# Kernel tuning notes

Hardware: AMD Instinct MI355X
Metric: run time of the kernel (lower is better)

Reference implementation:

```python
import jax, jax.numpy as jnp
import numpy as np

# Module config (init_kwargs)
K_PERIODS = 5
PMAX = 512
MIN_PERIOD_THRESHOLD = 2

B, T, N = 32, 2048, 128


def setup_inputs() -> dict:
    key = jax.random.key(0)
    x = jax.random.normal(key, (B, T, N), dtype=jnp.float32)
    return {"x": x}


def reference(x):
    """Faithful dense/padded JAX version of PeriodicityTransform.forward (mask=None).

    The torch module emits ragged PeriodGroups keyed by (cycles, period).
    Since jit requires static shapes, we return the same per-(series, freq)
    information in padded form:
      tiles   : [BN, K, T]  flattened folded tile (row-major cycle x period),
                 zero-padded past take = cycles*periods
      periods : [BN, K] int32
      cycles  : [BN, K] int32
    tiles[bn,k,:take].reshape(cycles, period) equals the torch tile exactly.
    """
    Bq, Tq, Nq = x.shape
    BN = Bq * Nq
    seqs = jnp.transpose(x, (0, 2, 1)).reshape(BN, Tq)  # [BN, T]

    # --- _topk_freq ---
    spec = jnp.fft.rfft(seqs, axis=-1)                   # [BN, T//2+1]
    mag2 = spec.real ** 2 + spec.imag ** 2
    mag2 = mag2.at[..., 0].set(0.0)                      # kill DC
    k = min(K_PERIODS, mag2.shape[-1] - 1)
    _, kidx = jax.lax.top_k(mag2, k)                     # [BN, K]
    kidx = jnp.maximum(kidx, 1).astype(jnp.int32)

    # --- period / cycle computation (valid_lengths == T, no mask) ---
    lengths = jnp.int32(Tq)
    periods = lengths // kidx                            # [BN, K]
    periods = jnp.minimum(periods, PMAX)
    min_period = min(MIN_PERIOD_THRESHOLD, Tq)
    periods = jnp.maximum(periods, min_period)
    periods = jnp.maximum(periods, 1)
    cycles = jnp.maximum(lengths // periods, 1)          # [BN, K]

    take = cycles * periods                              # [BN, K], <= T
    t = jnp.arange(Tq, dtype=jnp.int32)                  # [T]
    start = Tq - take                                    # [BN, K]
    gather_idx = jnp.clip(start[..., None] + t, 0, Tq - 1)  # [BN, K, T]
    valid = t[None, None, :] < take[..., None]           # [BN, K, T]

    src = jnp.broadcast_to(seqs[:, None, :], (BN, k, Tq))
    tiles = jnp.take_along_axis(src, gather_idx, axis=-1)
    tiles = jnp.where(valid, tiles, jnp.zeros((), dtype=tiles.dtype))
    return tiles, periods, cycles
```

## Files before the change

kernel.cpp:

```cpp
#include <hip/hip_runtime.h>

#define B_ 32
#define T_ 2048
#define N_ 128
#define K_ 5
#define BN_ (B_ * N_)
#define PMAX_ 512
#define MINP_ 2

static constexpr double PI_D = 3.14159265358979323846264338327950288;
static constexpr double S2_D = 0.70710678118654752440084436210485;

struct cd { double r, i; };

__device__ __forceinline__ void bf_w(cd& u, cd& v, double wr, double wi) {
    const double tr = v.r * wr - v.i * wi;
    const double ti = v.r * wi + v.i * wr;
    v.r = u.r - tr; v.i = u.i - ti;
    u.r += tr;      u.i += ti;
}
__device__ __forceinline__ void bf_1(cd& u, cd& v) {
    const double tr = v.r, ti = v.i;
    v.r = u.r - tr; v.i = u.i - ti;
    u.r += tr;      u.i += ti;
}
__device__ __forceinline__ void bf_mi(cd& u, cd& v) {
    const double tr = v.i, ti = -v.r;
    v.r = u.r - tr; v.i = u.i - ti;
    u.r += tr;      u.i += ti;
}
__device__ __forceinline__ int sw(int i) { return i ^ ((i >> 5) & 31); }

__global__ __launch_bounds__(256) void pt_twiddle(double2* __restrict__ tw) {
    const int m = blockIdx.x * 256 + threadIdx.x;
    if (m < 1024) {
        double s, c;
        sincos(-2.0 * PI_D * (double)m / 2048.0, &s, &c);
        tw[m] = make_double2(c, s);
    }
}

__global__ __launch_bounds__(256, 4) void pt_fft_tiles(const float* __restrict__ x,
                                                       float* __restrict__ out,
                                                       const double2* __restrict__ tw) {
    __shared__ double re[2048];
    __shared__ double im[2048];
    __shared__ double redv[8];
    __shared__ int    redi[8];
    __shared__ int    win2[2];
    __shared__ int    sh_take[2][K_];

    const int i0  = blockIdx.x;
    const int q   = ((i0 & 7) << 8) | (i0 >> 3);
    const int bn0 = q * 2;
    const int b   = bn0 >> 7;
    const int n   = bn0 & 127;
    const int tid = threadIdx.x;

    const float* xp = x + (size_t)b * T_ * N_ + n;
    float2 v[8];
#pragma unroll
    for (int m = 0; m < 8; ++m)
        v[m] = *(const float2*)(xp + (size_t)(tid + 256 * m) * N_);

#pragma unroll
    for (int m = 0; m < 8; ++m) {
        const int t = tid + 256 * m;
        const int p = sw((int)(__brev((unsigned)t) >> 21));
        re[p] = (double)v[m].x;
        im[p] = (double)v[m].y;
    }
    __syncthreads();

    {
        const int base = tid * 8;
        cd E[8];
#pragma unroll
        for (int j = 0; j < 8; ++j) { const int p = sw(base + j); E[j].r = re[p]; E[j].i = im[p]; }
        bf_1(E[0], E[1]); bf_1(E[2], E[3]); bf_1(E[4], E[5]); bf_1(E[6], E[7]);
        bf_1(E[0], E[2]); bf_mi(E[1], E[3]); bf_1(E[4], E[6]); bf_mi(E[5], E[7]);
        bf_1(E[0], E[4]); bf_w(E[1], E[5], S2_D, -S2_D);
        bf_mi(E[2], E[6]); bf_w(E[3], E[7], -S2_D, -S2_D);
#pragma unroll
        for (int j = 0; j < 8; ++j) { const int p = sw(base + j); re[p] = E[j].r; im[p] = E[j].i; }
    }
    __syncthreads();

#pragma unroll
    for (int r = 0; r < 2; ++r) {
        const int s    = 4 + 3 * r;
        const int h    = 1 << (s - 1);
        const int bq   = tid & (h - 1);
        const int g    = tid >> (s - 1);
        const int base = g * 8 * h + bq;
        const double2 w1  = tw[bq << (11 - s)];
        const double2 w2a = tw[bq << (10 - s)];
        const double2 w2b = tw[(bq + h) << (10 - s)];
        const double2 w30 = tw[bq << (9 - s)];
        const double2 w31 = tw[(bq + h) << (9 - s)];
        const double2 w32 = tw[(bq + 2 * h) << (9 - s)];
        const double2 w33 = tw[(bq + 3 * h) << (9 - s)];
        cd E[8];
#pragma unroll
        for (int j = 0; j < 8; ++j) { const int p = sw(base + j * h); E[j].r = re[p]; E[j].i = im[p]; }
        bf_w(E[0], E[1], w1.x, w1.y);   bf_w(E[2], E[3], w1.x, w1.y);
        bf_w(E[4], E[5], w1.x, w1.y);   bf_w(E[6], E[7], w1.x, w1.y);
        bf_w(E[0], E[2], w2a.x, w2a.y); bf_w(E[1], E[3], w2b.x, w2b.y);
        bf_w(E[4], E[6], w2a.x, w2a.y); bf_w(E[5], E[7], w2b.x, w2b.y);
        bf_w(E[0], E[4], w30.x, w30.y); bf_w(E[1], E[5], w31.x, w31.y);
        bf_w(E[2], E[6], w32.x, w32.y); bf_w(E[3], E[7], w33.x, w33.y);
#pragma unroll
        for (int j = 0; j < 8; ++j) { const int p = sw(base + j * h); re[p] = E[j].r; im[p] = E[j].i; }
        __syncthreads();
    }

#pragma unroll
    for (int u = 0; u < 2; ++u) {
        const int bb = tid + 256 * u;
        const double2 wA = tw[bb << 1];
        const double2 wB = tw[bb];
        const double2 wC = tw[bb + 512];
        const int p0 = sw(bb), p1 = sw(bb + 512), p2 = sw(bb + 1024), p3 = sw(bb + 1536);
        cd E0 = {re[p0], im[p0]}, E1 = {re[p1], im[p1]};
        cd E2 = {re[p2], im[p2]}, E3 = {re[p3], im[p3]};
        bf_w(E0, E1, wA.x, wA.y); bf_w(E2, E3, wA.x, wA.y);
        bf_w(E0, E2, wB.x, wB.y); bf_w(E1, E3, wC.x, wC.y);
        re[p0] = E0.r; im[p0] = E0.i; re[p1] = E1.r; im[p1] = E1.i;
        re[p2] = E2.r; im[p2] = E2.i; re[p3] = E3.r; im[p3] = E3.i;
    }
    __syncthreads();

    double magsA[4], magsB[4];
#pragma unroll
    for (int m = 0; m < 4; ++m) {
        const int k  = 1 + tid + 256 * m;
        const int nk = 2048 - k;
        const int pk = sw(k), pn = sw(nk);
        const double zr = re[pk], zi = im[pk];
        const double yr = re[pn], yi = im[pn];
        const double ar = zr + yr, ai = zi - yi;
        const double br = zi + yi, bi = yr - zr;
        magsA[m] = ar * ar + ai * ai;
        magsB[m] = br * br + bi * bi;
    }

    const int wid  = tid >> 6;
    const int lane = tid & 63;
    for (int it = 0; it < K_; ++it) {
        double bvA = -1.0; int biA = 1 << 30;
        double bvB = -1.0; int biB = 1 << 30;
#pragma unroll
        for (int m = 0; m < 4; ++m) {
            const int k = 1 + tid + 256 * m;
            if (magsA[m] > bvA || (magsA[m] == bvA && k < biA)) { bvA = magsA[m]; biA = k; }
            if (magsB[m] > bvB || (magsB[m] == bvB && k < biB)) { bvB = magsB[m]; biB = k; }
        }
#pragma unroll
        for (int off = 32; off > 0; off >>= 1) {
            double v2 = __shfl_down(bvA, off); int i2 = __shfl_down(biA, off);
            if (v2 > bvA || (v2 == bvA && i2 < biA)) { bvA = v2; biA = i2; }
            v2 = __shfl_down(bvB, off); i2 = __shfl_down(biB, off);
            if (v2 > bvB || (v2 == bvB && i2 < biB)) { bvB = v2; biB = i2; }
        }
        if (lane == 0) {
            redv[wid] = bvA; redi[wid] = biA;
            redv[4 + wid] = bvB; redi[4 + wid] = biB;
        }
        __syncthreads();
        if (tid < 2) {
            const int base = 4 * tid;
            double vb = redv[base]; int ib = redi[base];
#pragma unroll
            for (int w = 1; w < 4; ++w) {
                const double v1 = redv[base + w]; const int i1 = redi[base + w];
                if (v1 > vb || (v1 == vb && i1 < ib)) { vb = v1; ib = i1; }
            }
            win2[tid] = ib;
            int period = T_ / ib;
            if (period > PMAX_) period = PMAX_;
            if (period < MINP_) period = MINP_;
            const int cyc = T_ / period;
            sh_take[tid][it] = (period << 16) | (period * cyc);
        }
        __syncthreads();
        const int wA = win2[0], wB = win2[1];
#pragma unroll
        for (int m = 0; m < 4; ++m) {
            const int k = 1 + tid + 256 * m;
            if (k == wA) magsA[m] = -1.0;
            if (k == wB) magsB[m] = -1.0;
        }
    }

    const size_t TILES = (size_t)BN_ * K_ * T_;
    if (tid < 2 * K_) {
        const int s2 = tid / K_, k2 = tid % K_;
        const int pk   = sh_take[s2][k2];
        const int per  = pk >> 16;
        const int take = pk & 0xFFFF;
        out[TILES + (size_t)(bn0 + s2) * K_ + k2]                      = (float)per;
        out[TILES + (size_t)BN_ * K_ + (size_t)(bn0 + s2) * K_ + k2]   = (float)(take / per);
    }

    float* rowA = out + (size_t)bn0 * (K_ * T_);
#pragma unroll
    for (int s2 = 0; s2 < 2; ++s2) {
#pragma unroll
        for (int k = 0; k < K_; ++k) {
            const int take  = sh_take[s2][k] & 0xFFFF;
            const int start = T_ - take;
            float* dst = rowA + (size_t)(s2 * K_ + k) * T_;
#pragma unroll
            for (int m = 0; m < 8; ++m) {
                const int t   = tid + 256 * m;
                const bool lo = (t < start);
                const int p   = lo ? (t + take) : (t - start);
                const float val = lo ? 0.0f : (s2 ? v[m].y : v[m].x);
                __builtin_nontemporal_store(val, dst + p);
            }
        }
    }
}

extern "C" void kernel_launch(void* const* d_in, const int* in_sizes, int n_in,
                              void* d_out, int out_size, void* d_ws, size_t ws_size,
                              hipStream_t stream) {
    const float* x = (const float*)d_in[0];
    float* out = (float*)d_out;
    double2* tw = (double2*)d_ws;

    pt_twiddle<<<dim3(4), dim3(256), 0, stream>>>(tw);
    pt_fft_tiles<<<dim3(BN_ / 2), dim3(256), 0, stream>>>(x, out, tw);
}
```

Before: 237.8 us.

## Compute per-wave top-K candidates locally and merge once, removing per-iteration barriers

Instead of a block-wide argmax with two barriers per top-K iteration, each wavefront independently extracts its own top-5 candidates via shuffles and writes them to shared memory. Two threads then merge the 4x5 candidates per series to pick the global top-5. This removes ten __syncthreads in exchange for a small serial merge on two threads. The merge relies on the global top-5 always being contained in the union of the per-wave top-5 lists.

Measured after the change: 247.6 us. +4.1%, slower.

```diff
diff --git a/kernel.cpp b/kernel.cpp
--- a/kernel.cpp
+++ b/kernel.cpp
@@ -45,9 +45,8 @@
                                                        const double2* __restrict__ tw) {
     __shared__ double re[2048];
     __shared__ double im[2048];
-    __shared__ double redv[8];
-    __shared__ int    redi[8];
-    __shared__ int    win2[2];
+    __shared__ double wcv[2][4][K_];
+    __shared__ int    wck[2][4][K_];
     __shared__ int    sh_take[2][K_];
 
     const int i0  = blockIdx.x;
@@ -146,6 +145,7 @@
 
     const int wid  = tid >> 6;
     const int lane = tid & 63;
+#pragma unroll
     for (int it = 0; it < K_; ++it) {
         double bvA = -1.0; int biA = 1 << 30;
         double bvB = -1.0; int biB = 1 << 30;
@@ -162,35 +162,48 @@
             v2 = __shfl_down(bvB, off); i2 = __shfl_down(biB, off);
             if (v2 > bvB || (v2 == bvB && i2 < biB)) { bvB = v2; biB = i2; }
         }
+        const double wvA = __shfl(bvA, 0); const int wiA = __shfl(biA, 0);
+        const double wvB = __shfl(bvB, 0); const int wiB = __shfl(biB, 0);
         if (lane == 0) {
-            redv[wid] = bvA; redi[wid] = biA;
-            redv[4 + wid] = bvB; redi[4 + wid] = biB;
-        }
-        __syncthreads();
-        if (tid < 2) {
-            const int base = 4 * tid;
-            double vb = redv[base]; int ib = redi[base];
-#pragma unroll
-            for (int w = 1; w < 4; ++w) {
-                const double v1 = redv[base + w]; const int i1 = redi[base + w];
-                if (v1 > vb || (v1 == vb && i1 < ib)) { vb = v1; ib = i1; }
+            wcv[0][wid][it] = wvA; wck[0][wid][it] = wiA;
+            wcv[1][wid][it] = wvB; wck[1][wid][it] = wiB;
+        }
+#pragma unroll
+        for (int m = 0; m < 4; ++m) {
+            const int k = 1 + tid + 256 * m;
+            if (k == wiA) magsA[m] = -1.0;
+            if (k == wiB) magsB[m] = -1.0;
+        }
+    }
+    __syncthreads();
+
+    if (tid < 2) {
+        double cv[20]; int ck[20];
+#pragma unroll
+        for (int w = 0; w < 4; ++w)
+#pragma unroll
+            for (int j = 0; j < K_; ++j) {
+                cv[w * K_ + j] = wcv[tid][w][j];
+                ck[w * K_ + j] = wck[tid][w][j];
             }
-            win2[tid] = ib;
+        unsigned used = 0;
+#pragma unroll
+        for (int it = 0; it < K_; ++it) {
+            double vb = -2.0; int ib = 1 << 30; int sel = 0;
+#pragma unroll
+            for (int c = 0; c < 20; ++c) {
+                if (used & (1u << c)) continue;
+                if (cv[c] > vb || (cv[c] == vb && ck[c] < ib)) { vb = cv[c]; ib = ck[c]; sel = c; }
+            }
+            used |= (1u << sel);
             int period = T_ / ib;
             if (period > PMAX_) period = PMAX_;
             if (period < MINP_) period = MINP_;
             const int cyc = T_ / period;
             sh_take[tid][it] = (period << 16) | (period * cyc);
         }
-        __syncthreads();
-        const int wA = win2[0], wB = win2[1];
-#pragma unroll
-        for (int m = 0; m < 4; ++m) {
-            const int k = 1 + tid + 256 * m;
-            if (k == wA) magsA[m] = -1.0;
-            if (k == wB) magsB[m] = -1.0;
-        }
-    }
+    }
+    __syncthreads();
 
     const size_t TILES = (size_t)BN_ * K_ * T_;
     if (tid < 2 * K_) {
```
